# Kernel tuning notes

Measured on AMD Instinct MI355X. Metric: run time of the kernel, lower is better.

The kernel has to match this reference:

```python
import jax, jax.numpy as jnp
import numpy as np

NF = 256  # node_feat_size
GF = 256  # graph_feat_size
V = 262144
G = 4096


def setup_inputs() -> dict:
    key = jax.random.key(0)
    ks = jax.random.split(key, 12)
    node_feats = jax.random.normal(ks[0], (V, NF), dtype=jnp.float32)
    g_feats = jax.random.normal(ks[1], (G, GF), dtype=jnp.float32)
    segment_ids = jnp.sort(jax.random.randint(ks[2], (V,), 0, G, dtype=jnp.int32))
    s = 0.05
    # compute_logits: Linear(NF+GF -> 1)
    Wl = jax.random.normal(ks[3], (1, NF + GF), dtype=jnp.float32) * s
    bl = jnp.zeros((1,), dtype=jnp.float32)
    # project_nodes: Linear(NF -> GF)  (dropout=0 -> identity)
    Wp = jax.random.normal(ks[4], (GF, NF), dtype=jnp.float32) * s
    bp = jnp.zeros((GF,), dtype=jnp.float32)
    # GRUCell(GF, GF), torch gate order (r, z, n)
    W_ih = jax.random.normal(ks[5], (3 * GF, GF), dtype=jnp.float32) * s
    W_hh = jax.random.normal(ks[6], (3 * GF, GF), dtype=jnp.float32) * s
    b_ih = jnp.zeros((3 * GF,), dtype=jnp.float32)
    b_hh = jnp.zeros((3 * GF,), dtype=jnp.float32)
    return dict(node_feats=node_feats, g_feats=g_feats, segment_ids=segment_ids,
                Wl=Wl, bl=bl, Wp=Wp, bp=bp,
                W_ih=W_ih, W_hh=W_hh, b_ih=b_ih, b_hh=b_hh)


def reference(node_feats, g_feats, segment_ids, Wl, bl, Wp, bp, W_ih, W_hh, b_ih, b_hh):
    num_graphs = g_feats.shape[0]
    # broadcast relu(g_feats) to nodes, concat with node feats, logits Linear + LeakyReLU
    gb = jax.nn.relu(g_feats)[segment_ids]                      # [V, GF]
    cat = jnp.concatenate([gb, node_feats], axis=1)             # [V, GF+NF]
    z = jax.nn.leaky_relu(cat @ Wl.T + bl, negative_slope=0.01) # [V, 1]
    # segmented softmax over nodes per graph
    m = jax.ops.segment_max(z, segment_ids, num_segments=num_graphs,
                            indices_are_sorted=True)            # [G, 1]
    e = jnp.exp(z - m[segment_ids])                             # [V, 1]
    denom = jax.ops.segment_sum(e, segment_ids, num_segments=num_graphs,
                                indices_are_sorted=True)        # [G, 1]
    a = e / denom[segment_ids]                                  # [V, 1]
    # project nodes (dropout p=0 -> identity) and weighted sum per graph
    hv = node_feats @ Wp.T + bp                                 # [V, GF]
    context = jax.ops.segment_sum(a * hv, segment_ids, num_segments=num_graphs,
                                  indices_are_sorted=True)      # [G, GF]
    context = jax.nn.elu(context)
    # GRUCell: input=context, hidden=g_feats, torch gate order r,z,n
    gi = context @ W_ih.T + b_ih                                # [G, 3*GF]
    gh = g_feats @ W_hh.T + b_hh                                # [G, 3*GF]
    i_r, i_z, i_n = jnp.split(gi, 3, axis=1)
    h_r, h_z, h_n = jnp.split(gh, 3, axis=1)
    r = jax.nn.sigmoid(i_r + h_r)
    u = jax.nn.sigmoid(i_z + h_z)
    n = jnp.tanh(i_n + r * h_n)
    h_new = (1.0 - u) * n + u * g_feats
    return h_new
```

## Files before the change

### kernel.cpp

```cpp
#include <hip/hip_runtime.h>
#include <hip/hip_bf16.h>
#include <stdint.h>

typedef unsigned short u16;
typedef __attribute__((ext_vector_type(8))) short short8;
typedef __attribute__((ext_vector_type(4))) float floatx4;

#define NFEAT 256

__device__ __forceinline__ unsigned short f2b(float f) {
    unsigned int x = __builtin_bit_cast(unsigned int, f);
    x += 0x7fffu + ((x >> 16) & 1u);
    return (unsigned short)(x >> 16);
}
__device__ __forceinline__ float sigmoidf_(float x) {
    return 1.0f / (1.0f + __expf(-x));
}

__global__ void __launch_bounds__(256)
k1_attn_pool(const float* __restrict__ nf, const float* __restrict__ gf,
             const int* __restrict__ seg, const float* __restrict__ Wl,
             const float* __restrict__ bl,
             const float* __restrict__ Wp, const float* __restrict__ Wih,
             const float* __restrict__ Whh,
             float* __restrict__ zbuf, u16* __restrict__ s_out,
             float* __restrict__ pres, u16* __restrict__ gfb,
             u16* __restrict__ wpb, u16* __restrict__ wihb, u16* __restrict__ whhb,
             int V)
{
    const int g = blockIdx.x;
    const int t = threadIdx.x;
    __shared__ float red[256];

    {
        const int n1 = 256 * 256;
        const int n2 = n1 + 768 * 256;
        const int n3 = n2 + 768 * 256;
        int idx = g * 256 + t;
        if (idx < n3) {
            if (idx < n1)       wpb[idx]       = f2b(Wp[idx]);
            else if (idx < n2)  wihb[idx - n1] = f2b(Wih[idx - n1]);
            else                whhb[idx - n2] = f2b(Whh[idx - n2]);
        }
    }

    const float gfv = gf[(size_t)g * NFEAT + t];
    gfb[(size_t)g * NFEAT + t] = f2b(gfv);
    red[t] = fmaxf(gfv, 0.0f) * Wl[t];
    __syncthreads();
    #pragma unroll
    for (int off = 128; off > 0; off >>= 1) {
        if (t < off) red[t] += red[t + off];
        __syncthreads();
    }
    const float gbase = red[0] + bl[0];
    __syncthreads();

    int lo = 0, hi = V;
    while (lo < hi) { int mid = (lo + hi) >> 1; if (seg[mid] < g) lo = mid + 1; else hi = mid; }
    const int start = lo;
    hi = V;
    while (lo < hi) { int mid = (lo + hi) >> 1; if (seg[mid] <= g) lo = mid + 1; else hi = mid; }
    const int count = lo - start;

    const int lane = t & 63;
    const int wv = t >> 6;

    const float4 wn = *(const float4*)(Wl + NFEAT + lane * 4);

    for (int i = wv; i < count; i += 4) {
        const float4 rv = *(const float4*)(nf + (size_t)(start + i) * NFEAT + lane * 4);
        float d = rv.x * wn.x + rv.y * wn.y + rv.z * wn.z + rv.w * wn.w;
        #pragma unroll
        for (int off = 32; off > 0; off >>= 1) d += __shfl_xor(d, off);
        if (lane == 0) {
            float z = d + gbase;
            zbuf[start + i] = (z > 0.0f) ? z : 0.01f * z;
        }
    }
    __syncthreads();

    float m = -3.0e38f;
    for (int i = t; i < count; i += 256) m = fmaxf(m, zbuf[start + i]);
    red[t] = m;
    __syncthreads();
    #pragma unroll
    for (int off = 128; off > 0; off >>= 1) {
        if (t < off) red[t] = fmaxf(red[t], red[t + off]);
        __syncthreads();
    }
    m = red[0];
    __syncthreads();

    float ssum = 0.0f;
    for (int i = t; i < count; i += 256) ssum += __expf(zbuf[start + i] - m);
    red[t] = ssum;
    __syncthreads();
    #pragma unroll
    for (int off = 128; off > 0; off >>= 1) {
        if (t < off) red[t] += red[t + off];
        __syncthreads();
    }
    const float inv = 1.0f / red[0];
    __syncthreads();

    for (int i = t; i < count; i += 256)
        zbuf[start + i] = __expf(zbuf[start + i] - m) * inv;
    __syncthreads();

    float a0 = 0.f, a1 = 0.f, a2 = 0.f, a3 = 0.f;
    int i = 0;
    for (; i + 3 < count; i += 4) {
        float w0 = zbuf[start + i];
        float w1 = zbuf[start + i + 1];
        float w2 = zbuf[start + i + 2];
        float w3 = zbuf[start + i + 3];
        a0 += w0 * nf[(size_t)(start + i    ) * NFEAT + t];
        a1 += w1 * nf[(size_t)(start + i + 1) * NFEAT + t];
        a2 += w2 * nf[(size_t)(start + i + 2) * NFEAT + t];
        a3 += w3 * nf[(size_t)(start + i + 3) * NFEAT + t];
    }
    for (; i < count; ++i)
        a0 += zbuf[start + i] * nf[(size_t)(start + i) * NFEAT + t];
    s_out[(size_t)g * NFEAT + t] = f2b((a0 + a1) + (a2 + a3));
    if (t == 0) pres[g] = (count > 0) ? 1.0f : 0.0f;
}

__global__ void __launch_bounds__(256)
k2a_project(const u16* __restrict__ s, const u16* __restrict__ Wpb,
            const float* __restrict__ bp, const float* __restrict__ pres,
            u16* __restrict__ ctx)
{
    const int t = threadIdx.x;
    const int wid = blockIdx.x * 4 + (t >> 6);
    const int lane = t & 63;
    const int m0 = (wid >> 4) * 16;
    const int n0 = (wid & 15) * 16;
    const int lr = lane & 15;
    const int kh = lane >> 4;

    const short* A = (const short*)s   + (size_t)(m0 + lr) * NFEAT + kh * 8;
    const short* B = (const short*)Wpb + (size_t)(n0 + lr) * NFEAT + kh * 8;

    floatx4 acc = {0.f, 0.f, 0.f, 0.f};
    #pragma unroll
    for (int k = 0; k < NFEAT; k += 32) {
        short8 a = *(const short8*)(A + k);
        short8 b = *(const short8*)(B + k);
        acc = __builtin_amdgcn_mfma_f32_16x16x32_bf16(a, b, acc, 0, 0, 0);
    }
    const int col = n0 + lr;
    const float bias = bp[col];
    const int rbase = m0 + kh * 4;
    #pragma unroll
    for (int r = 0; r < 4; ++r) {
        int row = rbase + r;
        float x = acc[r] + bias * pres[row];
        x = (x > 0.0f) ? x : (__expf(x) - 1.0f);
        ctx[(size_t)row * NFEAT + col] = f2b(x);
    }
}

__global__ void __launch_bounds__(256)
k2b_gru(const u16* __restrict__ ctx, const u16* __restrict__ gfb,
        const float* __restrict__ gf,
        const u16* __restrict__ Wih, const u16* __restrict__ Whh,
        const float* __restrict__ bih, const float* __restrict__ bhh,
        float* __restrict__ out)
{
    const int t = threadIdx.x;
    const int wid = blockIdx.x * 4 + (t >> 6);
    const int lane = t & 63;
    const int m0 = (wid >> 4) * 16;
    const int j0 = (wid & 15) * 16;
    const int lr = lane & 15;
    const int kh = lane >> 4;

    const short* A1 = (const short*)ctx + (size_t)(m0 + lr) * NFEAT + kh * 8;
    const short* A2 = (const short*)gfb + (size_t)(m0 + lr) * NFEAT + kh * 8;
    const size_t boff = (size_t)(j0 + lr) * NFEAT + kh * 8;
    const short* Bir = (const short*)Wih + boff;
    const short* Biz = Bir + 256 * NFEAT;
    const short* Bin = Bir + 512 * NFEAT;
    const short* Bhr = (const short*)Whh + boff;
    const short* Bhz = Bhr + 256 * NFEAT;
    const short* Bhn = Bhr + 512 * NFEAT;

    floatx4 air = {0,0,0,0}, aiz = {0,0,0,0}, ain = {0,0,0,0};
    floatx4 ahr = {0,0,0,0}, ahz = {0,0,0,0}, ahn = {0,0,0,0};
    #pragma unroll
    for (int k = 0; k < NFEAT; k += 32) {
        short8 a1 = *(const short8*)(A1 + k);
        short8 a2 = *(const short8*)(A2 + k);
        air = __builtin_amdgcn_mfma_f32_16x16x32_bf16(a1, *(const short8*)(Bir + k), air, 0, 0, 0);
        aiz = __builtin_amdgcn_mfma_f32_16x16x32_bf16(a1, *(const short8*)(Biz + k), aiz, 0, 0, 0);
        ain = __builtin_amdgcn_mfma_f32_16x16x32_bf16(a1, *(const short8*)(Bin + k), ain, 0, 0, 0);
        ahr = __builtin_amdgcn_mfma_f32_16x16x32_bf16(a2, *(const short8*)(Bhr + k), ahr, 0, 0, 0);
        ahz = __builtin_amdgcn_mfma_f32_16x16x32_bf16(a2, *(const short8*)(Bhz + k), ahz, 0, 0, 0);
        ahn = __builtin_amdgcn_mfma_f32_16x16x32_bf16(a2, *(const short8*)(Bhn + k), ahn, 0, 0, 0);
    }
    const int col = j0 + lr;
    const float b_ir = bih[col], b_iz = bih[256 + col], b_in = bih[512 + col];
    const float b_hr = bhh[col], b_hz = bhh[256 + col], b_hn = bhh[512 + col];
    const int rbase = m0 + kh * 4;
    #pragma unroll
    for (int r = 0; r < 4; ++r) {
        int row = rbase + r;
        float rg = sigmoidf_((air[r] + b_ir) + (ahr[r] + b_hr));
        float ug = sigmoidf_((aiz[r] + b_iz) + (ahz[r] + b_hz));
        float ng = tanhf((ain[r] + b_in) + rg * (ahn[r] + b_hn));
        float h  = gf[(size_t)row * NFEAT + col];
        out[(size_t)row * NFEAT + col] = (1.0f - ug) * ng + ug * h;
    }
}

extern "C" void kernel_launch(void* const* d_in, const int* in_sizes, int n_in,
                              void* d_out, int out_size, void* d_ws, size_t ws_size,
                              hipStream_t stream)
{
    const float* nf  = (const float*)d_in[0];
    const float* gf  = (const float*)d_in[1];
    const int*   seg = (const int*)d_in[2];
    const float* Wl  = (const float*)d_in[3];
    const float* bl  = (const float*)d_in[4];
    const float* Wp  = (const float*)d_in[5];
    const float* bp  = (const float*)d_in[6];
    const float* Wih = (const float*)d_in[7];
    const float* Whh = (const float*)d_in[8];
    const float* bih = (const float*)d_in[9];
    const float* bhh = (const float*)d_in[10];

    const int V = in_sizes[2];
    const int G = in_sizes[1] / NFEAT;

    char* ws = (char*)d_ws;
    float* zbuf = (float*)ws;                         ws += (size_t)V * 4;
    u16*   sbuf = (u16*)ws;                           ws += (size_t)G * NFEAT * 2;
    u16*   ctx  = (u16*)ws;                           ws += (size_t)G * NFEAT * 2;
    u16*   gfb  = (u16*)ws;                           ws += (size_t)G * NFEAT * 2;
    u16*   wpb  = (u16*)ws;                           ws += (size_t)256 * 256 * 2;
    u16*   wihb = (u16*)ws;                           ws += (size_t)768 * 256 * 2;
    u16*   whhb = (u16*)ws;                           ws += (size_t)768 * 256 * 2;
    float* pres = (float*)ws;                         ws += (size_t)G * 4;

    k1_attn_pool<<<G, 256, 0, stream>>>(nf, gf, seg, Wl, bl, Wp, Wih, Whh,
                                        zbuf, sbuf, pres, gfb, wpb, wihb, whhb, V);
    k2a_project<<<G / 4, 256, 0, stream>>>(sbuf, wpb, bp, pres, ctx);
    k2b_gru<<<G / 4, 256, 0, stream>>>(ctx, gfb, gf, wihb, whhb, bih, bhh, (float*)d_out);
    (void)ws_size; (void)n_in; (void)out_size;
}
```

Baseline: 463.3 us.

## Fuse logits, segment softmax and weighted pooling into one-pass online softmax

Replaces the multi-pass attention pooling (write logits to a global buffer, reduce max, reduce sum, normalize, then re-read node features for the weighted sum) with a single streaming pass. Each wave keeps a running max, normalizer and weighted accumulator while reading each node row once. Per-wave partials are merged through shared memory at the end. The next row is also prefetched. This removes the second read of node features and the global z buffer, at the cost of extra exp work per node.

```diff
diff --git a/kernel.cpp b/kernel.cpp
--- a/kernel.cpp
+++ b/kernel.cpp
@@ -23,7 +23,7 @@
              const float* __restrict__ bl,
              const float* __restrict__ Wp, const float* __restrict__ Wih,
              const float* __restrict__ Whh,
-             float* __restrict__ zbuf, u16* __restrict__ s_out,
+             u16* __restrict__ s_out,
              float* __restrict__ pres, u16* __restrict__ gfb,
              u16* __restrict__ wpb, u16* __restrict__ wihb, u16* __restrict__ whhb,
              int V)
@@ -31,6 +31,8 @@
     const int g = blockIdx.x;
     const int t = threadIdx.x;
     __shared__ float red[256];
+    __shared__ float accs[4][256];
+    __shared__ float mws[4], lws[4];
 
     {
         const int n1 = 256 * 256;
@@ -68,61 +70,46 @@
 
     const float4 wn = *(const float4*)(Wl + NFEAT + lane * 4);
 
+    float m = -3.0e38f, l = 0.0f;
+    float4 acc = {0.f, 0.f, 0.f, 0.f};
+    const float* base = nf + (size_t)start * NFEAT + lane * 4;
+
+    float4 x = {0.f, 0.f, 0.f, 0.f};
+    if (wv < count) x = *(const float4*)(base + (size_t)wv * NFEAT);
     for (int i = wv; i < count; i += 4) {
-        const float4 rv = *(const float4*)(nf + (size_t)(start + i) * NFEAT + lane * 4);
-        float d = rv.x * wn.x + rv.y * wn.y + rv.z * wn.z + rv.w * wn.w;
+        float4 nx = {0.f, 0.f, 0.f, 0.f};
+        if (i + 4 < count) nx = *(const float4*)(base + (size_t)(i + 4) * NFEAT);
+        float d = x.x * wn.x + x.y * wn.y + x.z * wn.z + x.w * wn.w;
         #pragma unroll
         for (int off = 32; off > 0; off >>= 1) d += __shfl_xor(d, off);
-        if (lane == 0) {
-            float z = d + gbase;
-            zbuf[start + i] = (z > 0.0f) ? z : 0.01f * z;
-        }
-    }
+        float z = d + gbase;
+        z = (z > 0.0f) ? z : 0.01f * z;
+        float mn = fmaxf(m, z);
+        float c = __expf(m - mn);
+        float p = __expf(z - mn);
+        l = l * c + p;
+        acc.x = acc.x * c + p * x.x;
+        acc.y = acc.y * c + p * x.y;
+        acc.z = acc.z * c + p * x.z;
+        acc.w = acc.w * c + p * x.w;
+        m = mn;
+        x = nx;
+    }
+
+    accs[wv][lane * 4 + 0] = acc.x;
+    accs[wv][lane * 4 + 1] = acc.y;
+    accs[wv][lane * 4 + 2] = acc.z;
+    accs[wv][lane * 4 + 3] = acc.w;
+    if (lane == 0) { mws[wv] = m; lws[wv] = l; }
     __syncthreads();
 
-    float m = -3.0e38f;
-    for (int i = t; i < count; i += 256) m = fmaxf(m, zbuf[start + i]);
-    red[t] = m;
-    __syncthreads();
-    #pragma unroll
-    for (int off = 128; off > 0; off >>= 1) {
-        if (t < off) red[t] = fmaxf(red[t], red[t + off]);
-        __syncthreads();
-    }
-    m = red[0];
-    __syncthreads();
-
-    float ssum = 0.0f;
-    for (int i = t; i < count; i += 256) ssum += __expf(zbuf[start + i] - m);
-    red[t] = ssum;
-    __syncthreads();
-    #pragma unroll
-    for (int off = 128; off > 0; off >>= 1) {
-        if (t < off) red[t] += red[t + off];
-        __syncthreads();
-    }
-    const float inv = 1.0f / red[0];
-    __syncthreads();
-
-    for (int i = t; i < count; i += 256)
-        zbuf[start + i] = __expf(zbuf[start + i] - m) * inv;
-    __syncthreads();
-
-    float a0 = 0.f, a1 = 0.f, a2 = 0.f, a3 = 0.f;
-    int i = 0;
-    for (; i + 3 < count; i += 4) {
-        float w0 = zbuf[start + i];
-        float w1 = zbuf[start + i + 1];
-        float w2 = zbuf[start + i + 2];
-        float w3 = zbuf[start + i + 3];
-        a0 += w0 * nf[(size_t)(start + i    ) * NFEAT + t];
-        a1 += w1 * nf[(size_t)(start + i + 1) * NFEAT + t];
-        a2 += w2 * nf[(size_t)(start + i + 2) * NFEAT + t];
-        a3 += w3 * nf[(size_t)(start + i + 3) * NFEAT + t];
-    }
-    for (; i < count; ++i)
-        a0 += zbuf[start + i] * nf[(size_t)(start + i) * NFEAT + t];
-    s_out[(size_t)g * NFEAT + t] = f2b((a0 + a1) + (a2 + a3));
+    const float M = fmaxf(fmaxf(mws[0], mws[1]), fmaxf(mws[2], mws[3]));
+    const float c0 = __expf(mws[0] - M), c1 = __expf(mws[1] - M);
+    const float c2 = __expf(mws[2] - M), c3 = __expf(mws[3] - M);
+    const float L = lws[0] * c0 + lws[1] * c1 + lws[2] * c2 + lws[3] * c3;
+    const float sv = accs[0][t] * c0 + accs[1][t] * c1 + accs[2][t] * c2 + accs[3][t] * c3;
+    const float inv = (L > 0.0f) ? 1.0f / L : 0.0f;
+    s_out[(size_t)g * NFEAT + t] = f2b(sv * inv);
     if (t == 0) pres[g] = (count > 0) ? 1.0f : 0.0f;
 }
 
@@ -234,7 +221,6 @@
     const int G = in_sizes[1] / NFEAT;
 
     char* ws = (char*)d_ws;
-    float* zbuf = (float*)ws;                         ws += (size_t)V * 4;
     u16*   sbuf = (u16*)ws;                           ws += (size_t)G * NFEAT * 2;
     u16*   ctx  = (u16*)ws;                           ws += (size_t)G * NFEAT * 2;
     u16*   gfb  = (u16*)ws;                           ws += (size_t)G * NFEAT * 2;
@@ -244,7 +230,7 @@
     float* pres = (float*)ws;                         ws += (size_t)G * 4;
 
     k1_attn_pool<<<G, 256, 0, stream>>>(nf, gf, seg, Wl, bl, Wp, Wih, Whh,
-                                        zbuf, sbuf, pres, gfb, wpb, wihb, whhb, V);
+                                        sbuf, pres, gfb, wpb, wihb, whhb, V);
     k2a_project<<<G / 4, 256, 0, stream>>>(sbuf, wpb, bp, pres, ctx);
     k2b_gru<<<G / 4, 256, 0, stream>>>(ctx, gfb, gf, wihb, whhb, bih, bhh, (float*)d_out);
     (void)ws_size; (void)n_in; (void)out_size;
```

Result: faster. 438.1 us (-5.4%).
